# Optimization experiments

Measured on AMD Instinct MI355X. Metric: run time of the kernel, lower is better.

## Reference

```python
import jax, jax.numpy as jnp
import numpy as np

DIM = 512
HEADS = 8
DIM_HEAD = DIM // 8          # 64
INNER = HEADS * DIM_HEAD     # 512
M_LANDMARKS = DIM // 2       # 256
PINV_ITERS = 6
RES_KERNEL = 33
LN_EPS = 1e-5


def setup_inputs() -> dict:
    key = jax.random.key(0)
    ks = jax.random.split(key, 7)
    b, n = 8, 4096
    x = jax.random.normal(ks[0], (b, n, DIM), dtype=jnp.float32)
    gamma = jnp.ones((DIM,), jnp.float32)
    beta = jnp.zeros((DIM,), jnp.float32)
    w_qkv = jax.random.normal(ks[1], (DIM, 3 * INNER), jnp.float32) * 0.02
    w_out = jax.random.normal(ks[2], (INNER, DIM), jnp.float32) * 0.02
    b_out = jnp.zeros((DIM,), jnp.float32)
    # depthwise Conv2d(heads, heads, (33,1), groups=heads): torch weight [H,1,33,1]
    res_kernel = jax.random.normal(ks[3], (HEADS, 1, RES_KERNEL, 1), jnp.float32) * 0.05
    return {"x": x, "gamma": gamma, "beta": beta, "w_qkv": w_qkv,
            "w_out": w_out, "b_out": b_out, "res_kernel": res_kernel}


def _moore_penrose_pinv(a, iters=PINV_ITERS):
    # a: [b, h, m, m]
    abs_a = jnp.abs(a)
    col = abs_a.sum(axis=-1).max()   # global max, as in torch.max(col)
    row = abs_a.sum(axis=-2).max()
    z = jnp.swapaxes(a, -1, -2) / (col * row)
    I = jnp.eye(a.shape[-1], dtype=a.dtype)
    for _ in range(iters):
        az = a @ z
        z = 0.25 * z @ (13. * I - az @ (15. * I - az @ (7. * I - az)))
    return z


def _nystrom_attention(xn, w_qkv, res_kernel, w_out, b_out):
    b, n, _ = xn.shape
    h, dh, m = HEADS, DIM_HEAD, M_LANDMARKS
    scale = dh ** -0.5
    qkv = xn @ w_qkv                               # [b, n, 3*inner]
    q, k, v = jnp.split(qkv, 3, axis=-1)
    def to_heads(t):
        return t.reshape(b, n, h, dh).transpose(0, 2, 1, 3)  # [b,h,n,dh]
    q, k, v = to_heads(q), to_heads(k), to_heads(v)
    q = q * scale

    l = n // m  # n chosen as multiple of m -> no padding branch
    # landmark pooling: '(m l) d -> m d' mean
    q_l = q.reshape(b, h, m, l, dh).mean(axis=3)   # [b,h,m,dh]
    k_l = k.reshape(b, h, m, l, dh).mean(axis=3)

    sim1 = jnp.einsum('bhid,bhjd->bhij', q, k_l)    # [b,h,n,m]
    sim2 = jnp.einsum('bhid,bhjd->bhij', q_l, k_l)  # [b,h,m,m]
    sim3 = jnp.einsum('bhid,bhjd->bhij', q_l, k)    # [b,h,m,n]

    attn1 = jax.nn.softmax(sim1, axis=-1)
    attn2 = jax.nn.softmax(sim2, axis=-1)
    attn3 = jax.nn.softmax(sim3, axis=-1)

    attn2_inv = _moore_penrose_pinv(attn2)
    out = (attn1 @ attn2_inv) @ (attn3 @ v)         # [b,h,n,dh]

    # residual depthwise conv over sequence dim (kernel 33x1, groups=heads)
    pad = RES_KERNEL // 2
    out = out + jax.lax.conv_general_dilated(
        v, res_kernel, window_strides=(1, 1),
        padding=((pad, pad), (0, 0)),
        dimension_numbers=('NCHW', 'OIHW', 'NCHW'),
        feature_group_count=HEADS)

    out = out.transpose(0, 2, 1, 3).reshape(b, n, h * dh)  # [b,n,inner]
    return out @ w_out + b_out  # dropout omitted (eval mode)


def reference(x, gamma, beta, w_qkv, w_out, b_out, res_kernel):
    mu = x.mean(axis=-1, keepdims=True)
    var = x.var(axis=-1, keepdims=True)
    xn = (x - mu) * jax.lax.rsqrt(var + LN_EPS) * gamma + beta
    return x + _nystrom_attention(xn, w_qkv, res_kernel, w_out, b_out)
```

## Files before the change

kernel.cpp:

```cpp
#include <hip/hip_runtime.h>

#define SEQ 4096
#define DMODEL 512
#define NH 8
#define DH 64
#define MLM 256
#define NBH 64
#define NROWS 32768

typedef unsigned short bf16_t;
typedef __attribute__((ext_vector_type(8))) short bf16x8;
typedef __attribute__((ext_vector_type(4))) float f32x4;

__device__ __forceinline__ float bf2f(unsigned short u) {
  return __uint_as_float(((unsigned)u) << 16);
}
__device__ __forceinline__ unsigned short f2bf(float f) {
  unsigned u = __float_as_uint(f);
  u += 0x7fffu + ((u >> 16) & 1u);
  return (unsigned short)(u >> 16);
}
__device__ __forceinline__ void unp8(const bf16_t* p, float* d) {
  uint4 u = *(const uint4*)p;
  d[0] = __uint_as_float(u.x << 16); d[1] = __uint_as_float(u.x & 0xffff0000u);
  d[2] = __uint_as_float(u.y << 16); d[3] = __uint_as_float(u.y & 0xffff0000u);
  d[4] = __uint_as_float(u.z << 16); d[5] = __uint_as_float(u.z & 0xffff0000u);
  d[6] = __uint_as_float(u.w << 16); d[7] = __uint_as_float(u.w & 0xffff0000u);
}

__device__ __forceinline__ void gll(const void* g, void* l) {
  __builtin_amdgcn_global_load_lds(
      (const __attribute__((address_space(1))) unsigned int*)g,
      (__attribute__((address_space(3))) unsigned int*)l, 16, 0, 0);
}

__global__ __launch_bounds__(64) void ln_kernel(const float* __restrict__ x,
    const float* __restrict__ gamma, const float* __restrict__ beta,
    bf16_t* __restrict__ xn) {
  int row = blockIdx.x;
  const float4* xr = (const float4*)(x + (size_t)row * DMODEL);
  int t = threadIdx.x;
  float4 a = xr[t], b = xr[t + 64];
  float s  = a.x + a.y + a.z + a.w + b.x + b.y + b.z + b.w;
  float ss = a.x*a.x + a.y*a.y + a.z*a.z + a.w*a.w
           + b.x*b.x + b.y*b.y + b.z*b.z + b.w*b.w;
#pragma unroll
  for (int off = 32; off > 0; off >>= 1) {
    s  += __shfl_xor(s, off);
    ss += __shfl_xor(ss, off);
  }
  float mean = s * (1.0f / DMODEL);
  float var  = ss * (1.0f / DMODEL) - mean * mean;
  float rstd = rsqrtf(var + 1e-5f);
  const float4* g4 = (const float4*)gamma;
  const float4* be4 = (const float4*)beta;
  ushort4* o = (ushort4*)(xn + (size_t)row * DMODEL);
  float4 g = g4[t], bb = be4[t];
  ushort4 r;
  r.x = f2bf((a.x - mean) * rstd * g.x + bb.x);
  r.y = f2bf((a.y - mean) * rstd * g.y + bb.y);
  r.z = f2bf((a.z - mean) * rstd * g.z + bb.z);
  r.w = f2bf((a.w - mean) * rstd * g.w + bb.w);
  o[t] = r;
  g = g4[t + 64]; bb = be4[t + 64];
  r.x = f2bf((b.x - mean) * rstd * g.x + bb.x);
  r.y = f2bf((b.y - mean) * rstd * g.y + bb.y);
  r.z = f2bf((b.z - mean) * rstd * g.z + bb.z);
  r.w = f2bf((b.w - mean) * rstd * g.w + bb.w);
  o[t + 64] = r;
}

__global__ __launch_bounds__(256) void convT(const float* __restrict__ w,
    bf16_t* __restrict__ wt, int K, int N) {
  size_t idx = (size_t)blockIdx.x * 256 + threadIdx.x;
  int n = (int)(idx / K), k = (int)(idx % K);
  wt[idx] = f2bf(w[(size_t)k * N + n]);
}

#define MFMA_GEMM_BODY(APTR, BTPTR, KDIM) \
  __shared__ short As[128][32]; \
  __shared__ short Bs[128][32]; \
  int tid = threadIdx.x; \
  int lane = tid & 63; \
  int wv = tid >> 6; \
  int wm = (wv & 1) << 6, wn = (wv >> 1) << 6; \
  int l15 = lane & 15, l16 = lane >> 4; \
  f32x4 acc[4][4]; \
  _Pragma("unroll") for (int fm = 0; fm < 4; ++fm) \
    _Pragma("unroll") for (int fn = 0; fn < 4; ++fn) \
      acc[fm][fn] = (f32x4){0.f, 0.f, 0.f, 0.f}; \
  int ar0 = tid >> 2, ac0 = (tid & 3) << 3; \
  const bf16_t* Ab  = (APTR) + (size_t)(m0 + ar0) * (KDIM) + ac0; \
  const bf16_t* Ab1 = (APTR) + (size_t)(m0 + ar0 + 64) * (KDIM) + ac0; \
  const bf16_t* Bb  = (BTPTR) + (size_t)(n0 + ar0) * (KDIM) + ac0; \
  const bf16_t* Bb1 = (BTPTR) + (size_t)(n0 + ar0 + 64) * (KDIM) + ac0; \
  short* AsW  = &As[(wv << 4)][0]; \
  short* AsW1 = &As[64 + (wv << 4)][0]; \
  short* BsW  = &Bs[(wv << 4)][0]; \
  short* BsW1 = &Bs[64 + (wv << 4)][0]; \
  for (int k0 = 0; k0 < (KDIM); k0 += 32) { \
    gll(Ab + k0, AsW);  gll(Ab1 + k0, AsW1); \
    gll(Bb + k0, BsW);  gll(Bb1 + k0, BsW1); \
    __syncthreads(); \
    bf16x8 af[4], bfr[4]; \
    _Pragma("unroll") for (int f = 0; f < 4; ++f) { \
      af[f]  = *(const bf16x8*)&As[wm + f * 16 + l15][l16 * 8]; \
      bfr[f] = *(const bf16x8*)&Bs[wn + f * 16 + l15][l16 * 8]; \
    } \
    _Pragma("unroll") for (int fm = 0; fm < 4; ++fm) \
      _Pragma("unroll") for (int fn = 0; fn < 4; ++fn) \
        acc[fm][fn] = __builtin_amdgcn_mfma_f32_16x16x32_bf16(af[fm], bfr[fn], acc[fm][fn], 0, 0, 0); \
    __syncthreads(); \
  }

__global__ __launch_bounds__(512) void gemm_qkv_256(const bf16_t* __restrict__ A,
    const bf16_t* __restrict__ BT, bf16_t* __restrict__ q, bf16_t* __restrict__ k,
    bf16_t* __restrict__ vT, bf16_t* __restrict__ qlb, bf16_t* __restrict__ klb) {
  int bid = blockIdx.x;
  int orig = (bid & 7) * 96 + (bid >> 3);
  int n0 = (orig % 6) << 8;
  int m0 = (orig / 6) << 8;
  __shared__ short As[4][8192];
  __shared__ short Bs[4][8192];
  int tid = threadIdx.x;
  int lane = tid & 63;
  int wid = tid >> 6;
  int wr = wid >> 2, wc = wid & 3;
  int l15 = lane & 15, l16 = lane >> 4;
  int sl = (l16 ^ (l15 & 3)) << 3;
  int gr  = lane >> 2;
  int gcs = ((lane & 3) ^ ((lane >> 2) & 3)) << 3;
  f32x4 acc[8][4];
#pragma unroll
  for (int fm = 0; fm < 8; ++fm)
#pragma unroll
    for (int fn = 0; fn < 4; ++fn) acc[fm][fn] = (f32x4){0.f, 0.f, 0.f, 0.f};

#define STAGE(kt, s) { \
    _Pragma("unroll") for (int u = 0; u < 2; ++u) { \
      int r0 = (wid << 5) + (u << 4); \
      gll(A  + (size_t)(m0 + r0 + gr) * 512 + (kt) * 32 + gcs, &As[s][r0 << 5]); \
      gll(BT + (size_t)(n0 + r0 + gr) * 512 + (kt) * 32 + gcs, &Bs[s][r0 << 5]); \
    } }

  STAGE(0, 0) STAGE(1, 1) STAGE(2, 2)
  for (int t = 0; t < 16; ++t) {
    int s = t & 3;
    if (t < 14)       asm volatile("s_waitcnt vmcnt(8)" ::: "memory");
    else if (t == 14) asm volatile("s_waitcnt vmcnt(4)" ::: "memory");
    else              asm volatile("s_waitcnt vmcnt(0)" ::: "memory");
    __builtin_amdgcn_s_barrier();
    if (t + 3 < 16) STAGE(t + 3, ((t + 3) & 3))
    bf16x8 a[8], b[4];
#pragma unroll
    for (int fm = 0; fm < 8; ++fm)
      a[fm] = *(const bf16x8*)&As[s][(((wr << 7) + (fm << 4) + l15) << 5) + sl];
#pragma unroll
    for (int fn = 0; fn < 4; ++fn)
      b[fn] = *(const bf16x8*)&Bs[s][(((wc << 6) + (fn << 4) + l15) << 5) + sl];
    asm volatile("s_waitcnt lgkmcnt(0)" ::: "memory");
    __builtin_amdgcn_sched_barrier(0);
    __builtin_amdgcn_s_setprio(1);
#pragma unroll
    for (int fm = 0; fm < 8; ++fm)
#pragma unroll
      for (int fn = 0; fn < 4; ++fn)
        acc[fm][fn] = __builtin_amdgcn_mfma_f32_16x16x32_bf16(a[fm], b[fn], acc[fm][fn], 0, 0, 0);
    __builtin_amdgcn_s_setprio(0);
  }
#undef STAGE
#pragma unroll
  for (int fm = 0; fm < 8; ++fm) {
    int row0 = m0 + (wr << 7) + (fm << 4) + (l16 << 2);
    int bat = row0 >> 12;
    int nn0 = row0 & 4095;
    int lm  = nn0 >> 4;
#pragma unroll
    for (int fn = 0; fn < 4; ++fn) {
      int col = n0 + (wc << 6) + (fn << 4) + l15;
      int which = col >> 9;
      int hd = (col >> 6) & 7;
      int d  = col & 63;
      if (which == 2) {
        ushort4 pk;
        pk.x = f2bf(acc[fm][fn][0]); pk.y = f2bf(acc[fm][fn][1]);
        pk.z = f2bf(acc[fm][fn][2]); pk.w = f2bf(acc[fm][fn][3]);
        *(ushort4*)(vT + ((size_t)(bat * NH + hd) * DH + d) * SEQ + nn0) = pk;
      } else {
        bf16_t* dst = (which == 0) ? q : k;
        float scale = (which == 0) ? 0.125f : 1.f;
#pragma unroll
        for (int rg = 0; rg < 4; ++rg)
          dst[(((size_t)(bat * NH + hd)) * SEQ + nn0 + rg) * DH + d] = f2bf(acc[fm][fn][rg] * scale);
        float s = acc[fm][fn][0] + acc[fm][fn][1] + acc[fm][fn][2] + acc[fm][fn][3];
        s += __shfl_xor(s, 16);
        s += __shfl_xor(s, 32);
        if (l16 == 0) {
          bf16_t* pdst = (which == 0) ? qlb : klb;
          pdst[((size_t)(bat * NH + hd) * MLM + lm) * DH + d] = f2bf(s * scale * 0.0625f);
        }
      }
    }
  }
}

__global__ __launch_bounds__(256) void gemm_out_mfma(const bf16_t* __restrict__ A,
    const bf16_t* __restrict__ BT, const float* __restrict__ bias,
    const float* __restrict__ x, float* __restrict__ y) {
  int bid = blockIdx.x;
  int orig = (bid & 7) * 128 + (bid >> 3);
  int n0 = (orig & 3) << 7;
  int m0 = (orig >> 2) << 7;
  MFMA_GEMM_BODY(A, BT, 512)
#pragma unroll
  for (int fm = 0; fm < 4; ++fm) {
#pragma unroll
    for (int fn = 0; fn < 4; ++fn) {
      int col = n0 + wn + fn * 16 + l15;
      float bv = bias[col];
#pragma unroll
      for (int rg = 0; rg < 4; ++rg) {
        int row = m0 + wm + fm * 16 + l16 * 4 + rg;
        y[(size_t)row * DMODEL + col] = x[(size_t)row * DMODEL + col] + acc[fm][fn][rg] + bv;
      }
    }
  }
}

__global__ __launch_bounds__(256) void bmm_mfma32(const bf16_t* __restrict__ Ag,
    const bf16_t* __restrict__ BTg, bf16_t* __restrict__ Cb,
    bf16_t* __restrict__ CTb, float* __restrict__ Cf,
    int K, float alpha, float eA, float diagc, int flags) {
  int bid = blockIdx.x;
  int orig = (bid & 7) * 512 + (bid >> 3);
  int bh = orig >> 6;
  int tile = orig & 63;
  int n0 = (tile & 7) << 5;
  int m0 = (tile >> 3) << 5;
  const bf16_t* A  = Ag + (size_t)bh * 256 * K;
  const bf16_t* BT = BTg + (size_t)bh * 256 * K;
  __shared__ short As[32][264];
  __shared__ short Bs[32][264];
  int tid = threadIdx.x;
  int lane = tid & 63;
  int wv = tid >> 6;
  int wm = (wv & 1) << 4, wn = (wv >> 1) << 4;
  int l15 = lane & 15, l16 = lane >> 4;
  int ar0 = tid >> 3, ac0 = (tid & 7) << 2;
  const bf16_t* Ab = A + (size_t)(m0 + ar0) * K + ac0;
  const bf16_t* Bb = BT + (size_t)(n0 + ar0) * K + ac0;
  int nch = K >> 5;
  uint2 ga[8], gb[8];
#pragma unroll 8
  for (int u = 0; u < 8; ++u)
    if (u < nch) { ga[u] = *(const uint2*)(Ab + u * 32); gb[u] = *(const uint2*)(Bb + u * 32); }
#pragma unroll 8
  for (int u = 0; u < 8; ++u)
    if (u < nch) { *(uint2*)&As[ar0][ac0 + u * 32] = ga[u]; *(uint2*)&Bs[ar0][ac0 + u * 32] = gb[u]; }
  __syncthreads();
  f32x4 acc = (f32x4){0.f, 0.f, 0.f, 0.f};
#pragma unroll 8
  for (int u = 0; u < 8; ++u)
    if (u < nch) {
      bf16x8 af = *(const bf16x8*)&As[wm + l15][u * 32 + l16 * 8];
      bf16x8 bf = *(const bf16x8*)&Bs[wn + l15][u * 32 + l16 * 8];
      acc = __builtin_amdgcn_mfma_f32_16x16x32_bf16(af, bf, acc, 0, 0, 0);
    }
  size_t cbase = (size_t)bh * 65536;
  int row0 = m0 + wm + l16 * 4;
  int col = n0 + wn + l15;
  float v4[4];
#pragma unroll
  for (int rg = 0; rg < 4; ++rg) {
    float val = alpha * acc[rg];
    if (eA != 0.f) val += eA * bf2f(A[(size_t)(row0 + rg) * K + col]);
    if (row0 + rg == col) val += diagc;
    v4[rg] = val;
  }
  if (flags & 1) {
#pragma unroll
    for (int rg = 0; rg < 4; ++rg)
      Cb[cbase + (size_t)(row0 + rg) * 256 + col] = f2bf(v4[rg]);
  }
  if (flags & 2) {
    ushort4 pk;
    pk.x = f2bf(v4[0]); pk.y = f2bf(v4[1]);
    pk.z = f2bf(v4[2]); pk.w = f2bf(v4[3]);
    *(ushort4*)(CTb + cbase + (size_t)col * 256 + row0) = pk;
  }
  if (flags & 4) {
#pragma unroll
    for (int rg = 0; rg < 4; ++rg)
      Cf[cbase + (size_t)(row0 + rg) * 256 + col] = v4[rg];
  }
}

__global__ __launch_bounds__(256) void ns_zy32(const bf16_t* __restrict__ zg,
    const bf16_t* __restrict__ Yg, const bf16_t* __restrict__ t1Tg,
    bf16_t* __restrict__ zog, bf16_t* __restrict__ Yog,
    bf16_t* __restrict__ YTog) {
  int bid = blockIdx.x;
  int orig = (bid & 7) * 1024 + (bid >> 3);
  int task = orig >> 6;
  int bh = task >> 1;
  int which = task & 1;
  int tile = orig & 63;
  int n0 = (tile & 7) << 5;
  int m0 = (tile >> 3) << 5;
  const bf16_t* A  = (which ? Yg : zg) + ((size_t)bh << 16);
  const bf16_t* BT = t1Tg + ((size_t)bh << 16);
  __shared__ short As[32][264];
  __shared__ short Bs[32][264];
  int tid = threadIdx.x;
  int lane = tid & 63;
  int wv = tid >> 6;
  int wm = (wv & 1) << 4, wn = (wv >> 1) << 4;
  int l15 = lane & 15, l16 = lane >> 4;
  int ar0 = tid >> 3, ac0 = (tid & 7) << 2;
  const bf16_t* Ab = A + (size_t)(m0 + ar0) * 256 + ac0;
  const bf16_t* Bb = BT + (size_t)(n0 + ar0) * 256 + ac0;
  uint2 ga[8], gb[8];
#pragma unroll
  for (int u = 0; u < 8; ++u) {
    ga[u] = *(const uint2*)(Ab + u * 32);
    gb[u] = *(const uint2*)(Bb + u * 32);
  }
#pragma unroll
  for (int u = 0; u < 8; ++u) {
    *(uint2*)&As[ar0][ac0 + u * 32] = ga[u];
    *(uint2*)&Bs[ar0][ac0 + u * 32] = gb[u];
  }
  __syncthreads();
  f32x4 acc = (f32x4){0.f, 0.f, 0.f, 0.f};
#pragma unroll
  for (int u = 0; u < 8; ++u) {
    bf16x8 af = *(const bf16x8*)&As[wm + l15][u * 32 + l16 * 8];
    bf16x8 bf = *(const bf16x8*)&Bs[wn + l15][u * 32 + l16 * 8];
    acc = __builtin_amdgcn_mfma_f32_16x16x32_bf16(af, bf, acc, 0, 0, 0);
  }
  size_t cbase = (size_t)bh << 16;
  int row0 = m0 + wm + l16 * 4;
  int col = n0 + wn + l15;
  float v4[4];
#pragma unroll
  for (int rg = 0; rg < 4; ++rg) v4[rg] = 0.25f * acc[rg];
  if (which == 0) {
#pragma unroll
    for (int rg = 0; rg < 4; ++rg)
      zog[cbase + (size_t)(row0 + rg) * 256 + col] = f2bf(v4[rg]);
  } else {
#pragma unroll
    for (int rg = 0; rg < 4; ++rg)
      Yog[cbase + (size_t)(row0 + rg) * 256 + col] = f2bf(v4[rg]);
    ushort4 pk;
    pk.x = f2bf(v4[0]); pk.y = f2bf(v4[1]);
    pk.z = f2bf(v4[2]); pk.w = f2bf(v4[3]);
    *(ushort4*)(YTog + cbase + (size_t)col * 256 + row0) = pk;
  }
}

__global__ __launch_bounds__(256) void softmax256(const float* __restrict__ af,
    bf16_t* __restrict__ ab) {
  const float* ar = af + (size_t)blockIdx.x * MLM;
  int t = threadIdx.x;
  float v = ar[t];
  __shared__ float redm[4], reds[4];
  float m = v;
#pragma unroll
  for (int off = 32; off > 0; off >>= 1) m = fmaxf(m, __shfl_xor(m, off));
  if ((t & 63) == 0) redm[t >> 6] = m;
  __syncthreads();
  m = fmaxf(fmaxf(redm[0], redm[1]), fmaxf(redm[2], redm[3]));
  float p = __expf(v - m);
  float s = p;
#pragma unroll
  for (int off = 32; off > 0; off >>= 1) s += __shfl_xor(s, off);
  if ((t & 63) == 0) reds[t >> 6] = s;
  __syncthreads();
  s = reds[0] + reds[1] + reds[2] + reds[3];
  ab[(size_t)blockIdx.x * MLM + t] = f2bf(p / s);
}

__global__ void init_scal(unsigned* s) { if (threadIdx.x < 2) s[threadIdx.x] = 0u; }

__global__ __launch_bounds__(256) void colrow_max(const bf16_t* __restrict__ a,
    unsigned* __restrict__ scal) {
  int bh = blockIdx.x;
  int task = blockIdx.y;
  const bf16_t* ab = a + (size_t)bh * MLM * MLM;
  int t = threadIdx.x;
  float s = 0.f;
  if (task == 0) {
    const bf16_t* rp = ab + (size_t)t * MLM;
    for (int j = 0; j < MLM; j += 8) {
      float d[8];
      unp8(rp + j, d);
      s += d[0]; s += d[1]; s += d[2]; s += d[3];
      s += d[4]; s += d[5]; s += d[6]; s += d[7];
    }
  } else {
    for (int i = 0; i < MLM; ++i) s += bf2f(ab[(size_t)i * MLM + t]);
  }
  __shared__ float red[4];
  float m = s;
#pragma unroll
  for (int off = 32; off > 0; off >>= 1) m = fmaxf(m, __shfl_xor(m, off));
  if ((t & 63) == 0) red[t >> 6] = m;
  __syncthreads();
  if (t == 0) {
    m = fmaxf(fmaxf(red[0], red[1]), fmaxf(red[2], red[3]));
    atomicMax(scal + task, __float_as_uint(m));
  }
}

__global__ __launch_bounds__(256) void zinit(const bf16_t* __restrict__ ab,
    bf16_t* __restrict__ z0, bf16_t* __restrict__ z0T,
    const unsigned* __restrict__ scal) {
  size_t idx = (size_t)blockIdx.x * 256 + threadIdx.x;
  float denom = __uint_as_float(scal[0]) * __uint_as_float(scal[1]);
  size_t bh = idx >> 16;
  int i = (int)((idx >> 8) & 255);
  int j = (int)(idx & 255);
  bf16_t r = f2bf(bf2f(ab[idx]) / denom);
  z0T[idx] = r;
  z0[(bh << 16) + ((size_t)j << 8) + i] = r;
}

__global__ __launch_bounds__(64) void attn3v_mfma(const bf16_t* __restrict__ qlb,
    const bf16_t* __restrict__ kg, const bf16_t* __restrict__ vT,
    float* __restrict__ pacc, float* __restrict__ pm, float* __restrict__ ps) {
  int bid = blockIdx.x;
  int orig = (bid & 7) * 512 + (bid >> 3);
  int m0 = (orig & 7) << 5;
  int cz = (orig >> 3) & 7;
  int bh = orig >> 6;
  int lane = threadIdx.x;
  int l15 = lane & 15, l16 = lane >> 4;
  __shared__ short plds[32][136];
  const bf16_t* qbase = qlb + (size_t)bh * MLM * DH;
  const bf16_t* kbase = kg + (size_t)bh * SEQ * DH;
  const bf16_t* vbase = vT + (size_t)bh * DH * SEQ;
  bf16x8 af[2][2];
#pragma unroll
  for (int mt = 0; mt < 2; ++mt)
#pragma unroll
    for (int ks = 0; ks < 2; ++ks)
      af[mt][ks] = *(const bf16x8*)(qbase + (size_t)(m0 + mt * 16 + l15) * DH + ks * 32 + l16 * 8);
  float m_run[2][4], s_run[2][4];
  f32x4 o[2][4];
#pragma unroll
  for (int mt = 0; mt < 2; ++mt) {
#pragma unroll
    for (int rg = 0; rg < 4; ++rg) { m_run[mt][rg] = -1e30f; s_run[mt][rg] = 0.f; }
#pragma unroll
    for (int n2 = 0; n2 < 4; ++n2) o[mt][n2] = (f32x4){0.f, 0.f, 0.f, 0.f};
  }
  int kbeg = cz << 9;
  for (int kt = kbeg; kt < kbeg + 512; kt += 128) {
    f32x4 sacc[2][8];
#pragma unroll
    for (int mt = 0; mt < 2; ++mt)
#pragma unroll
      for (int nt = 0; nt < 8; ++nt) sacc[mt][nt] = (f32x4){0.f, 0.f, 0.f, 0.f};
#pragma unroll
    for (int nt = 0; nt < 8; ++nt) {
      const bf16_t* kr = kbase + (size_t)(kt + nt * 16 + l15) * DH + l16 * 8;
      bf16x8 b0 = *(const bf16x8*)kr;
      bf16x8 b1 = *(const bf16x8*)(kr + 32);
      sacc[0][nt] = __builtin_amdgcn_mfma_f32_16x16x32_bf16(af[0][0], b0, sacc[0][nt], 0, 0, 0);
      sacc[0][nt] = __builtin_amdgcn_mfma_f32_16x16x32_bf16(af[0][1], b1, sacc[0][nt], 0, 0, 0);
      sacc[1][nt] = __builtin_amdgcn_mfma_f32_16x16x32_bf16(af[1][0], b0, sacc[1][nt], 0, 0, 0);
      sacc[1][nt] = __builtin_amdgcn_mfma_f32_16x16x32_bf16(af[1][1], b1, sacc[1][nt], 0, 0, 0);
    }
#pragma unroll
    for (int mt = 0; mt < 2; ++mt)
#pragma unroll
      for (int rg = 0; rg < 4; ++rg) {
        float mx = sacc[mt][0][rg];
#pragma unroll
        for (int nt = 1; nt < 8; ++nt) mx = fmaxf(mx, sacc[mt][nt][rg]);
        mx = fmaxf(mx, __shfl_xor(mx, 1));
        mx = fmaxf(mx, __shfl_xor(mx, 2));
        mx = fmaxf(mx, __shfl_xor(mx, 4));
        mx = fmaxf(mx, __shfl_xor(mx, 8));
        float mnew = fmaxf(m_run[mt][rg], mx);
        float corr = __expf(m_run[mt][rg] - mnew);
        float s = 0.f;
#pragma unroll
        for (int nt = 0; nt < 8; ++nt) {
          float p = __expf(sacc[mt][nt][rg] - mnew);
          sacc[mt][nt][rg] = p;
          s += p;
        }
        s += __shfl_xor(s, 1); s += __shfl_xor(s, 2);
        s += __shfl_xor(s, 4); s += __shfl_xor(s, 8);
        s_run[mt][rg] = s_run[mt][rg] * corr + s;
        m_run[mt][rg] = mnew;
#pragma unroll
        for (int n2 = 0; n2 < 4; ++n2) o[mt][n2][rg] *= corr;
      }
#pragma unroll
    for (int mt = 0; mt < 2; ++mt)
#pragma unroll
      for (int nt = 0; nt < 8; ++nt)
#pragma unroll
        for (int rg = 0; rg < 4; ++rg)
          plds[mt * 16 + l16 * 4 + rg][nt * 16 + l15] = (short)f2bf(sacc[mt][nt][rg]);
#pragma unroll
    for (int ks2 = 0; ks2 < 4; ++ks2) {
      bf16x8 pa0 = *(const bf16x8*)&plds[l15][ks2 * 32 + l16 * 8];
      bf16x8 pa1 = *(const bf16x8*)&plds[16 + l15][ks2 * 32 + l16 * 8];
#pragma unroll
      for (int n2 = 0; n2 < 4; ++n2) {
        bf16x8 vb8 = *(const bf16x8*)(vbase + (size_t)(n2 * 16 + l15) * SEQ + kt + ks2 * 32 + l16 * 8);
        o[0][n2] = __builtin_amdgcn_mfma_f32_16x16x32_bf16(pa0, vb8, o[0][n2], 0, 0, 0);
        o[1][n2] = __builtin_amdgcn_mfma_f32_16x16x32_bf16(pa1, vb8, o[1][n2], 0, 0, 0);
      }
    }
  }
  size_t pidx0 = (size_t)(bh * 8 + cz) * MLM + m0;
#pragma unroll
  for (int mt = 0; mt < 2; ++mt)
#pragma unroll
    for (int n2 = 0; n2 < 4; ++n2)
#pragma unroll
      for (int rg = 0; rg < 4; ++rg) {
        int row = mt * 16 + l16 * 4 + rg;
        pacc[(pidx0 + row) * 64 + n2 * 16 + l15] = o[mt][n2][rg];
      }
  if (l15 == 0) {
#pragma unroll
    for (int mt = 0; mt < 2; ++mt)
#pragma unroll
      for (int rg = 0; rg < 4; ++rg) {
        pm[pidx0 + mt * 16 + l16 * 4 + rg] = m_run[mt][rg];
        ps[pidx0 + mt * 16 + l16 * 4 + rg] = s_run[mt][rg];
      }
  }
}

__global__ __launch_bounds__(256) void attn3v_comb(const float* __restrict__ pacc,
    const float* __restrict__ pm, const float* __restrict__ ps,
    bf16_t* __restrict__ a3vb) {
  int gw = blockIdx.x * 4 + (threadIdx.x >> 6);
  int lane = threadIdx.x & 63;
  int bh = gw >> 8, row = gw & 255;
  float ms[8];
  float M = -1e30f;
#pragma unroll
  for (int cc = 0; cc < 8; ++cc) {
    ms[cc] = pm[(size_t)(bh * 8 + cc) * MLM + row];
    M = fmaxf(M, ms[cc]);
  }
  float S = 0.f, val = 0.f;
#pragma unroll
  for (int cc = 0; cc < 8; ++cc) {
    size_t pidx = (size_t)(bh * 8 + cc) * MLM + row;
    float w = __expf(ms[cc] - M);
    S += w * ps[pidx];
    val += w * pacc[pidx * 64 + lane];
  }
  a3vb[(size_t)gw * 64 + lane] = f2bf(val / S);
}

__global__ __launch_bounds__(256) void wm_kernel(const bf16_t* __restrict__ zb,
    const bf16_t* __restrict__ a3vb, bf16_t* __restrict__ wmT) {
  int bh = blockIdx.y;
  int m0 = blockIdx.x << 6;
  __shared__ bf16_t a3s[MLM * DH];
  int t = threadIdx.x;
  const bf16_t* asrc = a3vb + (size_t)bh * MLM * DH;
#pragma unroll
  for (int i = 0; i < 8; ++i)
    *(bf16x8*)(a3s + ((size_t)t + 256 * i) * 8) =
        *(const bf16x8*)(asrc + ((size_t)t + 256 * i) * 8);
  __syncthreads();
  int row = m0 + (t >> 2);
  int c0 = (t & 3) * 16;
  const bf16_t* zrow = zb + (size_t)bh * 65536 + (size_t)row * 256;
  float acc16[16] = {};
  for (int k0 = 0; k0 < 256; k0 += 8) {
    float a8[8];
    unp8(zrow + k0, a8);
#pragma unroll
    for (int j = 0; j < 8; ++j) {
      float av[16];
      unp8(a3s + (k0 + j) * 64 + c0, av);
      unp8(a3s + (k0 + j) * 64 + c0 + 8, av + 8);
#pragma unroll
      for (int e = 0; e < 16; ++e) acc16[e] += a8[j] * av[e];
    }
  }
  bf16_t* wd = wmT + (size_t)bh * DH * MLM;
#pragma unroll
  for (int e = 0; e < 16; ++e)
    wd[(size_t)(c0 + e) * MLM + row] = f2bf(acc16[e]);
}

__global__ __launch_bounds__(64) void attn1_mfma(const bf16_t* __restrict__ qg,
    const bf16_t* __restrict__ klb, const bf16_t* __restrict__ wmT,
    bf16_t* __restrict__ om) {
  int bh = blockIdx.y, bat = bh >> 3, head = bh & 7;
  int m0 = blockIdx.x << 5;
  int lane = threadIdx.x;
  int l15 = lane & 15, l16 = lane >> 4;
  __shared__ short plds[32][264];
  const bf16_t* qbase = qg + (size_t)bh * SEQ * DH;
  const bf16_t* kbase = klb + (size_t)bh * MLM * DH;
  bf16x8 af[2][2];
#pragma unroll
  for (int mt = 0; mt < 2; ++mt)
#pragma unroll
    for (int ks = 0; ks < 2; ++ks)
      af[mt][ks] = *(const bf16x8*)(qbase + (size_t)(m0 + mt * 16 + l15) * DH + ks * 32 + l16 * 8);
  f32x4 acc[2][16];
#pragma unroll
  for (int mt = 0; mt < 2; ++mt)
#pragma unroll
    for (int nt = 0; nt < 16; ++nt) acc[mt][nt] = (f32x4){0.f, 0.f, 0.f, 0.f};
#pragma unroll
  for (int nt = 0; nt < 16; ++nt) {
    bf16x8 b0 = *(const bf16x8*)(kbase + (size_t)(nt * 16 + l15) * DH + l16 * 8);
    bf16x8 b1 = *(const bf16x8*)(kbase + (size_t)(nt * 16 + l15) * DH + 32 + l16 * 8);
    acc[0][nt] = __builtin_amdgcn_mfma_f32_16x16x32_bf16(af[0][0], b0, acc[0][nt], 0, 0, 0);
    acc[0][nt] = __builtin_amdgcn_mfma_f32_16x16x32_bf16(af[0][1], b1, acc[0][nt], 0, 0, 0);
    acc[1][nt] = __builtin_amdgcn_mfma_f32_16x16x32_bf16(af[1][0], b0, acc[1][nt], 0, 0, 0);
    acc[1][nt] = __builtin_amdgcn_mfma_f32_16x16x32_bf16(af[1][1], b1, acc[1][nt], 0, 0, 0);
  }
  float inv[2][4];
#pragma unroll
  for (int mt = 0; mt < 2; ++mt)
#pragma unroll
    for (int rg = 0; rg < 4; ++rg) {
      float mx = acc[mt][0][rg];
#pragma unroll
      for (int nt = 1; nt < 16; ++nt) mx = fmaxf(mx, acc[mt][nt][rg]);
      mx = fmaxf(mx, __shfl_xor(mx, 1));
      mx = fmaxf(mx, __shfl_xor(mx, 2));
      mx = fmaxf(mx, __shfl_xor(mx, 4));
      mx = fmaxf(mx, __shfl_xor(mx, 8));
      float s = 0.f;
#pragma unroll
      for (int nt = 0; nt < 16; ++nt) {
        float p = __expf(acc[mt][nt][rg] - mx);
        acc[mt][nt][rg] = p;
        s += p;
      }
      s += __shfl_xor(s, 1); s += __shfl_xor(s, 2);
      s += __shfl_xor(s, 4); s += __shfl_xor(s, 8);
      inv[mt][rg] = 1.f / s;
    }
#pragma unroll
  for (int mt = 0; mt < 2; ++mt)
#pragma unroll
    for (int nt = 0; nt < 16; ++nt)
#pragma unroll
      for (int rg = 0; rg < 4; ++rg)
        plds[mt * 16 + l16 * 4 + rg][nt * 16 + l15] = (short)f2bf(acc[mt][nt][rg]);
  const bf16_t* wbase = wmT + (size_t)bh * DH * MLM;
  f32x4 o[2][4];
#pragma unroll
  for (int mt = 0; mt < 2; ++mt)
#pragma unroll
    for (int n2 = 0; n2 < 4; ++n2) o[mt][n2] = (f32x4){0.f, 0.f, 0.f, 0.f};
#pragma unroll
  for (int ks = 0; ks < 8; ++ks) {
    bf16x8 pa0 = *(const bf16x8*)&plds[l15][ks * 32 + l16 * 8];
    bf16x8 pa1 = *(const bf16x8*)&plds[16 + l15][ks * 32 + l16 * 8];
#pragma unroll
    for (int n2 = 0; n2 < 4; ++n2) {
      bf16x8 wb = *(const bf16x8*)(wbase + (size_t)(n2 * 16 + l15) * MLM + ks * 32 + l16 * 8);
      o[0][n2] = __builtin_amdgcn_mfma_f32_16x16x32_bf16(pa0, wb, o[0][n2], 0, 0, 0);
      o[1][n2] = __builtin_amdgcn_mfma_f32_16x16x32_bf16(pa1, wb, o[1][n2], 0, 0, 0);
    }
  }
#pragma unroll
  for (int mt = 0; mt < 2; ++mt)
#pragma unroll
    for (int n2 = 0; n2 < 4; ++n2)
#pragma unroll
      for (int rg = 0; rg < 4; ++rg) {
        int n = m0 + mt * 16 + l16 * 4 + rg;
        int d = n2 * 16 + l15;
        om[((size_t)(bat * SEQ + n)) * DMODEL + head * DH + d] =
            f2bf(o[mt][n2][rg] * inv[mt][rg]);
      }
}

__global__ __launch_bounds__(256) void conv_add(const bf16_t* __restrict__ vT,
    const float* __restrict__ rk, bf16_t* __restrict__ om) {
  int bh = blockIdx.y, bat = bh >> 3, head = bh & 7;
  int n0 = blockIdx.x << 5;
  __shared__ bf16_t vs[64 * 64];
  int t = threadIdx.x;
  int d = t & 63;
  int nq = (t >> 6) << 4;
  const bf16_t* vrow = vT + ((size_t)bh * DH + d) * SEQ;
#pragma unroll
  for (int h = 0; h < 2; ++h) {
    int nb = n0 - 16 + nq + h * 8;
    unsigned short tmp[8];
    if (nb >= 0 && nb + 8 <= SEQ) {
      bf16x8 val = *(const bf16x8*)(vrow + nb);
#pragma unroll
      for (int e = 0; e < 8; ++e) tmp[e] = ((unsigned short*)&val)[e];
    } else {
#pragma unroll
      for (int e = 0; e < 8; ++e) {
        int n = nb + e;
        tmp[e] = (n >= 0 && n < SEQ) ? vrow[n] : (unsigned short)0;
      }
    }
#pragma unroll
    for (int e = 0; e < 8; ++e) vs[(nq + h * 8 + e) * 64 + d] = tmp[e];
  }
  __syncthreads();
  float w[33];
#pragma unroll
  for (int i = 0; i < 33; ++i) w[i] = rk[head * 33 + i];
  int r0 = (t >> 6) << 3;
  float out[8] = {0.f, 0.f, 0.f, 0.f, 0.f, 0.f, 0.f, 0.f};
#pragma unroll
  for (int j = 0; j < 40; ++j) {
    float vv = bf2f(vs[(r0 + j) * 64 + d]);
    int ilo = j - 32; if (ilo < 0) ilo = 0;
    int ihi = j; if (ihi > 7) ihi = 7;
    for (int i = ilo; i <= ihi; ++i) out[i] += w[j - i] * vv;
  }
#pragma unroll
  for (int i = 0; i < 8; ++i) {
    int n = n0 + r0 + i;
    size_t idx = ((size_t)(bat * SEQ + n)) * DMODEL + head * DH + d;
    om[idx] = f2bf(bf2f(om[idx]) + out[i]);
  }
}

extern "C" void kernel_launch(void* const* d_in, const int* in_sizes, int n_in,
                              void* d_out, int out_size, void* d_ws, size_t ws_size,
                              hipStream_t stream) {
  const float* x     = (const float*)d_in[0];
  const float* gamma = (const float*)d_in[1];
  const float* beta  = (const float*)d_in[2];
  const float* w_qkv = (const float*)d_in[3];
  const float* w_out = (const float*)d_in[4];
  const float* b_out = (const float*)d_in[5];
  const float* rk    = (const float*)d_in[6];
  float* y  = (float*)d_out;

  bf16_t* xnb  = (bf16_t*)d_ws;
  bf16_t* qb   = xnb + 16777216;
  bf16_t* kb   = qb + 16777216;
  bf16_t* vTb  = kb + 16777216;
  bf16_t* wqkvT = vTb + 16777216;
  bf16_t* woutT = wqkvT + 786432;
  bf16_t* qlb  = woutT + 262144;
  bf16_t* klb  = qlb + 1048576;
  bf16_t* a2b  = klb + 1048576;
  bf16_t* zA   = a2b + 4194304;
  bf16_t* z0T  = zA + 4194304;
  bf16_t* zB   = z0T + 4194304;
  bf16_t* Ya   = zB + 4194304;
  bf16_t* Yb   = z0T;
  bf16_t* a3vb = Ya + 4194304;
  bf16_t* wmT  = a3vb + 1048576;
  float*  SR   = (float*)(wmT + 1048576);
  float*  a2f  = SR;
  float*  pacc = SR;
  bf16_t* YTa  = (bf16_t*)SR;
  bf16_t* YTb  = YTa + 4194304;
  bf16_t* t2T  = YTa + 8388608;
  bf16_t* t1T  = YTa + 12582912;
  float*  pm   = SR + 8388608;
  float*  ps   = pm + 131072;
  unsigned* scal = (unsigned*)(ps + 131072);
  size_t need = (size_t)93323264 * 2 + (size_t)(8388608 + 262144) * 4 + 64;
  if (ws_size < need) return;

  ln_kernel<<<NROWS, 64, 0, stream>>>(x, gamma, beta, xnb);
  convT<<<3072, 256, 0, stream>>>(w_qkv, wqkvT, 512, 1536);
  convT<<<1024, 256, 0, stream>>>(w_out, woutT, 512, 512);

  gemm_qkv_256<<<768, 512, 0, stream>>>(xnb, wqkvT, qb, kb, vTb, qlb, klb);

  bmm_mfma32<<<4096, 256, 0, stream>>>(qlb, klb, nullptr, nullptr, a2f,
      64, 1.f, 0.f, 0.f, 4);
  softmax256<<<NBH * MLM, 256, 0, stream>>>(a2f, a2b);

  init_scal<<<1, 64, 0, stream>>>(scal);
  colrow_max<<<dim3(NBH, 2), 256, 0, stream>>>(a2b, scal);

  attn3v_mfma<<<4096, 64, 0, stream>>>(qlb, kb, vTb, pacc, pm, ps);
  attn3v_comb<<<4096, 256, 0, stream>>>(pacc, pm, ps, a3vb);

  zinit<<<16384, 256, 0, stream>>>(a2b, zA, z0T, scal);
  bmm_mfma32<<<4096, 256, 0, stream>>>(a2b, z0T, Ya, YTa, nullptr,
      256, 1.f, 0.f, 0.f, 3);
  bf16_t* zc = zA;  bf16_t* zo = zB;
  bf16_t* Yc = Ya;  bf16_t* YTc = YTa;
  bf16_t* Yo = Yb;  bf16_t* YTo = YTb;
  for (int it = 0; it < 6; ++it) {
    bmm_mfma32<<<4096, 256, 0, stream>>>(Yc, YTc, nullptr, t2T, nullptr,
        256, 1.f, -7.f, 15.f, 2);
    bmm_mfma32<<<4096, 256, 0, stream>>>(Yc, t2T, nullptr, t1T, nullptr,
        256, -1.f, 0.f, 13.f, 2);
    ns_zy32<<<8192, 256, 0, stream>>>(zc, Yc, t1T, zo, Yo, YTo);
    bf16_t* tp;
    tp = zc; zc = zo; zo = tp;
    tp = Yc; Yc = Yo; Yo = tp;
    tp = YTc; YTc = YTo; YTo = tp;
  }

  wm_kernel<<<dim3(4, NBH), 256, 0, stream>>>(zc, a3vb, wmT);

  bf16_t* om = xnb;
  attn1_mfma<<<dim3(SEQ / 32, NBH), 64, 0, stream>>>(qb, klb, wmT, om);
  conv_add<<<dim3(SEQ / 32, NBH), 256, 0, stream>>>(vTb, rk, om);

  gemm_out_mfma<<<1024, 256, 0, stream>>>(om, woutT, b_out, x, y);
}
```

Before: 762.8 us.

## Restructure Newton-Schulz pinv iteration to pair independent GEMMs and defer z update

Rewrites each pseudo-inverse iteration so the Y update is expressed through W=Y·Y and U=7Y−W. The z update from the previous iteration (z·t1) runs alongside W in one launch, and Y·U and Y·U-based t1 run together in a second launch. That gives two launches per iteration instead of three, plus one final z GEMM. It also folds init_scal into the weight transpose kernel and zinit into the attn3v combine kernel to cut launch count. The change alters the bf16 rounding points in the iteration, which may shift numerics slightly.

```diff
diff --git a/kernel.cpp b/kernel.cpp
--- a/kernel.cpp
+++ b/kernel.cpp
@@ -70,11 +70,19 @@
   o[t + 64] = r;
 }
 
-__global__ __launch_bounds__(256) void convT(const float* __restrict__ w,
-    bf16_t* __restrict__ wt, int K, int N) {
+__global__ __launch_bounds__(256) void convT2(const float* __restrict__ wqkv,
+    const float* __restrict__ wout, bf16_t* __restrict__ wqkvT,
+    bf16_t* __restrict__ woutT, unsigned* __restrict__ scal) {
+  if (blockIdx.x == 0 && threadIdx.x < 2) scal[threadIdx.x] = 0u;
   size_t idx = (size_t)blockIdx.x * 256 + threadIdx.x;
-  int n = (int)(idx / K), k = (int)(idx % K);
-  wt[idx] = f2bf(w[(size_t)k * N + n]);
+  if (idx < 786432) {
+    int n = (int)(idx / 512), k = (int)(idx % 512);
+    wqkvT[idx] = f2bf(wqkv[(size_t)k * 1536 + n]);
+  } else {
+    size_t j = idx - 786432;
+    int n = (int)(j / 512), k = (int)(j % 512);
+    woutT[j] = f2bf(wout[(size_t)k * 512 + n]);
+  }
 }
 
 #define MFMA_GEMM_BODY(APTR, BTPTR, KDIM) \
@@ -112,6 +120,29 @@
         acc[fm][fn] = __builtin_amdgcn_mfma_f32_16x16x32_bf16(af[fm], bfr[fn], acc[fm][fn], 0, 0, 0); \
     __syncthreads(); \
   }
+
+#define BMM256_BODY(APTR, BTPTR) \
+  __shared__ short As[32][264]; \
+  __shared__ short Bs[32][264]; \
+  int tid = threadIdx.x; \
+  int lane = tid & 63; \
+  int wv = tid >> 6; \
+  int wm = (wv & 1) << 4, wn = (wv >> 1) << 4; \
+  int l15 = lane & 15, l16 = lane >> 4; \
+  int ar0 = tid >> 3, ac0 = (tid & 7) << 2; \
+  const bf16_t* Ab = (APTR) + (size_t)(m0 + ar0) * 256 + ac0; \
+  const bf16_t* Bb = (BTPTR) + (size_t)(n0 + ar0) * 256 + ac0; \
+  uint2 ga[8], gb[8]; \
+  _Pragma("unroll") for (int u = 0; u < 8; ++u) { \
+    ga[u] = *(const uint2*)(Ab + u * 32); gb[u] = *(const uint2*)(Bb + u * 32); } \
+  _Pragma("unroll") for (int u = 0; u < 8; ++u) { \
+    *(uint2*)&As[ar0][ac0 + u * 32] = ga[u]; *(uint2*)&Bs[ar0][ac0 + u * 32] = gb[u]; } \
+  __syncthreads(); \
+  f32x4 acc = (f32x4){0.f, 0.f, 0.f, 0.f}; \
+  _Pragma("unroll") for (int u = 0; u < 8; ++u) { \
+    bf16x8 af = *(const bf16x8*)&As[wm + l15][u * 32 + l16 * 8]; \
+    bf16x8 bf = *(const bf16x8*)&Bs[wn + l15][u * 32 + l16 * 8]; \
+    acc = __builtin_amdgcn_mfma_f32_16x16x32_bf16(af, bf, acc, 0, 0, 0); }
 
 __global__ __launch_bounds__(512) void gemm_qkv_256(const bf16_t* __restrict__ A,
     const bf16_t* __restrict__ BT, bf16_t* __restrict__ q, bf16_t* __restrict__ k,
@@ -295,67 +326,88 @@
   }
 }
 
-__global__ __launch_bounds__(256) void ns_zy32(const bf16_t* __restrict__ zg,
-    const bf16_t* __restrict__ Yg, const bf16_t* __restrict__ t1Tg,
-    bf16_t* __restrict__ zog, bf16_t* __restrict__ Yog,
-    bf16_t* __restrict__ YTog) {
+__global__ __launch_bounds__(256) void pinv_WU(const bf16_t* __restrict__ Yc,
+    const bf16_t* __restrict__ YTc, const bf16_t* __restrict__ zc,
+    const bf16_t* __restrict__ t1Tp, bf16_t* __restrict__ Wb,
+    bf16_t* __restrict__ UT, bf16_t* __restrict__ zo) {
   int bid = blockIdx.x;
-  int orig = (bid & 7) * 1024 + (bid >> 3);
-  int task = orig >> 6;
-  int bh = task >> 1;
-  int which = task & 1;
-  int tile = orig & 63;
+  int cpx = gridDim.x >> 3;
+  int orig = (bid & 7) * cpx + (bid >> 3);
+  int zt = orig >> 12;
+  int o = orig & 4095;
+  int bh = o >> 6;
+  int tile = o & 63;
   int n0 = (tile & 7) << 5;
   int m0 = (tile >> 3) << 5;
-  const bf16_t* A  = (which ? Yg : zg) + ((size_t)bh << 16);
-  const bf16_t* BT = t1Tg + ((size_t)bh << 16);
-  __shared__ short As[32][264];
-  __shared__ short Bs[32][264];
-  int tid = threadIdx.x;
-  int lane = tid & 63;
-  int wv = tid >> 6;
-  int wm = (wv & 1) << 4, wn = (wv >> 1) << 4;
-  int l15 = lane & 15, l16 = lane >> 4;
-  int ar0 = tid >> 3, ac0 = (tid & 7) << 2;
-  const bf16_t* Ab = A + (size_t)(m0 + ar0) * 256 + ac0;
-  const bf16_t* Bb = BT + (size_t)(n0 + ar0) * 256 + ac0;
-  uint2 ga[8], gb[8];
-#pragma unroll
-  for (int u = 0; u < 8; ++u) {
-    ga[u] = *(const uint2*)(Ab + u * 32);
-    gb[u] = *(const uint2*)(Bb + u * 32);
-  }
-#pragma unroll
-  for (int u = 0; u < 8; ++u) {
-    *(uint2*)&As[ar0][ac0 + u * 32] = ga[u];
-    *(uint2*)&Bs[ar0][ac0 + u * 32] = gb[u];
-  }
-  __syncthreads();
-  f32x4 acc = (f32x4){0.f, 0.f, 0.f, 0.f};
-#pragma unroll
-  for (int u = 0; u < 8; ++u) {
-    bf16x8 af = *(const bf16x8*)&As[wm + l15][u * 32 + l16 * 8];
-    bf16x8 bf = *(const bf16x8*)&Bs[wn + l15][u * 32 + l16 * 8];
-    acc = __builtin_amdgcn_mfma_f32_16x16x32_bf16(af, bf, acc, 0, 0, 0);
-  }
+  const bf16_t* A  = (zt ? zc : Yc) + ((size_t)bh << 16);
+  const bf16_t* BT = (zt ? t1Tp : YTc) + ((size_t)bh << 16);
+  BMM256_BODY(A, BT)
   size_t cbase = (size_t)bh << 16;
   int row0 = m0 + wm + l16 * 4;
   int col = n0 + wn + l15;
-  float v4[4];
-#pragma unroll
-  for (int rg = 0; rg < 4; ++rg) v4[rg] = 0.25f * acc[rg];
-  if (which == 0) {
+  if (zt) {
 #pragma unroll
     for (int rg = 0; rg < 4; ++rg)
-      zog[cbase + (size_t)(row0 + rg) * 256 + col] = f2bf(v4[rg]);
+      zo[cbase + (size_t)(row0 + rg) * 256 + col] = f2bf(0.25f * acc[rg]);
   } else {
-#pragma unroll
-    for (int rg = 0; rg < 4; ++rg)
-      Yog[cbase + (size_t)(row0 + rg) * 256 + col] = f2bf(v4[rg]);
     ushort4 pk;
-    pk.x = f2bf(v4[0]); pk.y = f2bf(v4[1]);
-    pk.z = f2bf(v4[2]); pk.w = f2bf(v4[3]);
-    *(ushort4*)(YTog + cbase + (size_t)col * 256 + row0) = pk;
+    unsigned short uv[4];
+#pragma unroll
+    for (int rg = 0; rg < 4; ++rg) {
+      float w = acc[rg];
+      float y = bf2f(Yc[cbase + (size_t)(row0 + rg) * 256 + col]);
+      Wb[cbase + (size_t)(row0 + rg) * 256 + col] = f2bf(w);
+      uv[rg] = f2bf(7.f * y - w);
+    }
+    pk.x = uv[0]; pk.y = uv[1]; pk.z = uv[2]; pk.w = uv[3];
+    *(ushort4*)(UT + cbase + (size_t)col * 256 + row0) = pk;
+  }
+}
+
+__global__ __launch_bounds__(256) void pinv_E(const bf16_t* __restrict__ Yc,
+    const bf16_t* __restrict__ Wb, const bf16_t* __restrict__ UT,
+    bf16_t* __restrict__ Yo, bf16_t* __restrict__ YTo,
+    bf16_t* __restrict__ t1T) {
+  int bid = blockIdx.x;
+  int orig = (bid & 7) * 1024 + (bid >> 3);
+  int task = orig >> 12;
+  int o = orig & 4095;
+  int bh = o >> 6;
+  int tile = o & 63;
+  int n0 = (tile & 7) << 5;
+  int m0 = (tile >> 3) << 5;
+  const bf16_t* A  = (task ? Yc : Wb) + ((size_t)bh << 16);
+  const bf16_t* BT = UT + ((size_t)bh << 16);
+  BMM256_BODY(A, BT)
+  size_t cbase = (size_t)bh << 16;
+  int row0 = m0 + wm + l16 * 4;
+  int col = n0 + wn + l15;
+  if (task == 0) {
+    ushort4 pk;
+    unsigned short yv[4];
+#pragma unroll
+    for (int rg = 0; rg < 4; ++rg) {
+      size_t idx = cbase + (size_t)(row0 + rg) * 256 + col;
+      float y = bf2f(Yc[idx]);
+      float w = bf2f(Wb[idx]);
+      float v = 0.25f * acc[rg] + 3.25f * y - 3.75f * w;
+      yv[rg] = f2bf(v);
+      Yo[idx] = yv[rg];
+    }
+    pk.x = yv[0]; pk.y = yv[1]; pk.z = yv[2]; pk.w = yv[3];
+    *(ushort4*)(YTo + cbase + (size_t)col * 256 + row0) = pk;
+  } else {
+    ushort4 pk;
+    unsigned short tv[4];
+#pragma unroll
+    for (int rg = 0; rg < 4; ++rg) {
+      float y = bf2f(Yc[cbase + (size_t)(row0 + rg) * 256 + col]);
+      float v = acc[rg] - 15.f * y;
+      if (row0 + rg == col) v += 13.f;
+      tv[rg] = f2bf(v);
+    }
+    pk.x = tv[0]; pk.y = tv[1]; pk.z = tv[2]; pk.w = tv[3];
+    *(ushort4*)(t1T + cbase + (size_t)col * 256 + row0) = pk;
   }
 }
 
@@ -380,8 +432,6 @@
   s = reds[0] + reds[1] + reds[2] + reds[3];
   ab[(size_t)blockIdx.x * MLM + t] = f2bf(p / s);
 }
-
-__global__ void init_scal(unsigned* s) { if (threadIdx.x < 2) s[threadIdx.x] = 0u; }
 
 __global__ __launch_bounds__(256) void colrow_max(const bf16_t* __restrict__ a,
     unsigned* __restrict__ scal) {
@@ -411,19 +461,6 @@
     m = fmaxf(fmaxf(red[0], red[1]), fmaxf(red[2], red[3]));
     atomicMax(scal + task, __float_as_uint(m));
   }
-}
-
-__global__ __launch_bounds__(256) void zinit(const bf16_t* __restrict__ ab,
-    bf16_t* __restrict__ z0, bf16_t* __restrict__ z0T,
-    const unsigned* __restrict__ scal) {
-  size_t idx = (size_t)blockIdx.x * 256 + threadIdx.x;
-  float denom = __uint_as_float(scal[0]) * __uint_as_float(scal[1]);
-  size_t bh = idx >> 16;
-  int i = (int)((idx >> 8) & 255);
-  int j = (int)(idx & 255);
-  bf16_t r = f2bf(bf2f(ab[idx]) / denom);
-  z0T[idx] = r;
-  z0[(bh << 16) + ((size_t)j << 8) + i] = r;
 }
 
 __global__ __launch_bounds__(64) void attn3v_mfma(const bf16_t* __restrict__ qlb,
@@ -539,28 +576,41 @@
   }
 }
 
-__global__ __launch_bounds__(256) void attn3v_comb(const float* __restrict__ pacc,
+__global__ __launch_bounds__(256) void comb_zinit(const float* __restrict__ pacc,
     const float* __restrict__ pm, const float* __restrict__ ps,
-    bf16_t* __restrict__ a3vb) {
-  int gw = blockIdx.x * 4 + (threadIdx.x >> 6);
-  int lane = threadIdx.x & 63;
-  int bh = gw >> 8, row = gw & 255;
-  float ms[8];
-  float M = -1e30f;
-#pragma unroll
-  for (int cc = 0; cc < 8; ++cc) {
-    ms[cc] = pm[(size_t)(bh * 8 + cc) * MLM + row];
-    M = fmaxf(M, ms[cc]);
-  }
-  float S = 0.f, val = 0.f;
-#pragma unroll
-  for (int cc = 0; cc < 8; ++cc) {
-    size_t pidx = (size_t)(bh * 8 + cc) * MLM + row;
-    float w = __expf(ms[cc] - M);
-    S += w * ps[pidx];
-    val += w * pacc[pidx * 64 + lane];
-  }
-  a3vb[(size_t)gw * 64 + lane] = f2bf(val / S);
+    bf16_t* __restrict__ a3vb, const bf16_t* __restrict__ ab,
+    bf16_t* __restrict__ z0, bf16_t* __restrict__ z0T,
+    const unsigned* __restrict__ scal) {
+  if (blockIdx.x < 4096) {
+    int gw = blockIdx.x * 4 + (threadIdx.x >> 6);
+    int lane = threadIdx.x & 63;
+    int bh = gw >> 8, row = gw & 255;
+    float ms[8];
+    float M = -1e30f;
+#pragma unroll
+    for (int cc = 0; cc < 8; ++cc) {
+      ms[cc] = pm[(size_t)(bh * 8 + cc) * MLM + row];
+      M = fmaxf(M, ms[cc]);
+    }
+    float S = 0.f, val = 0.f;
+#pragma unroll
+    for (int cc = 0; cc < 8; ++cc) {
+      size_t pidx = (size_t)(bh * 8 + cc) * MLM + row;
+      float w = __expf(ms[cc] - M);
+      S += w * ps[pidx];
+      val += w * pacc[pidx * 64 + lane];
+    }
+    a3vb[(size_t)gw * 64 + lane] = f2bf(val / S);
+  } else {
+    size_t idx = (size_t)(blockIdx.x - 4096) * 256 + threadIdx.x;
+    float denom = __uint_as_float(scal[0]) * __uint_as_float(scal[1]);
+    size_t bh = idx >> 16;
+    int i = (int)((idx >> 8) & 255);
+    int j = (int)(idx & 255);
+    bf16_t r = f2bf(bf2f(ab[idx]) / denom);
+    z0T[idx] = r;
+    z0[(bh << 16) + ((size_t)j << 8) + i] = r;
+  }
 }
 
 __global__ __launch_bounds__(256) void wm_kernel(const bf16_t* __restrict__ zb,
@@ -768,8 +818,9 @@
   float*  pacc = SR;
   bf16_t* YTa  = (bf16_t*)SR;
   bf16_t* YTb  = YTa + 4194304;
-  bf16_t* t2T  = YTa + 8388608;
+  bf16_t* Wb   = YTa + 8388608;
   bf16_t* t1T  = YTa + 12582912;
+  bf16_t* UT   = xnb;
   float*  pm   = SR + 8388608;
   float*  ps   = pm + 131072;
   unsigned* scal = (unsigned*)(ps + 131072);
@@ -777,38 +828,39 @@
   if (ws_size < need) return;
 
   ln_kernel<<<NROWS, 64, 0, stream>>>(x, gamma, beta, xnb);
-  convT<<<3072, 256, 0, stream>>>(w_qkv, wqkvT, 512, 1536);
-  convT<<<1024, 256, 0, stream>>>(w_out, woutT, 512, 512);
+  convT2<<<4096, 256, 0, stream>>>(w_qkv, w_out, wqkvT, woutT, scal);
 
   gemm_qkv_256<<<768, 512, 0, stream>>>(xnb, wqkvT, qb, kb, vTb, qlb, klb);
 
   bmm_mfma32<<<4096, 256, 0, stream>>>(qlb, klb, nullptr, nullptr, a2f,
       64, 1.f, 0.f, 0.f, 4);
   softmax256<<<NBH * MLM, 256, 0, stream>>>(a2f, a2b);
-
-  init_scal<<<1, 64, 0, stream>>>(scal);
   colrow_max<<<dim3(NBH, 2), 256, 0, stream>>>(a2b, scal);
 
   attn3v_mfma<<<4096, 64, 0, stream>>>(qlb, kb, vTb, pacc, pm, ps);
-  attn3v_comb<<<4096, 256, 0, stream>>>(pacc, pm, ps, a3vb);
-
-  zinit<<<16384, 256, 0, stream>>>(a2b, zA, z0T, scal);
+  comb_zinit<<<20480, 256, 0, stream>>>(pacc, pm, ps, a3vb, a2b, zA, z0T, scal);
+
   bmm_mfma32<<<4096, 256, 0, stream>>>(a2b, z0T, Ya, YTa, nullptr,
       256, 1.f, 0.f, 0.f, 3);
+
   bf16_t* zc = zA;  bf16_t* zo = zB;
   bf16_t* Yc = Ya;  bf16_t* YTc = YTa;
   bf16_t* Yo = Yb;  bf16_t* YTo = YTb;
   for (int it = 0; it < 6; ++it) {
-    bmm_mfma32<<<4096, 256, 0, stream>>>(Yc, YTc, nullptr, t2T, nullptr,
-        256, 1.f, -7.f, 15.f, 2);
-    bmm_mfma32<<<4096, 256, 0, stream>>>(Yc, t2T, nullptr, t1T, nullptr,
-        256, -1.f, 0.f, 13.f, 2);
-    ns_zy32<<<8192, 256, 0, stream>>>(zc, Yc, t1T, zo, Yo, YTo);
+    if (it == 0) {
+      pinv_WU<<<4096, 256, 0, stream>>>(Yc, YTc, nullptr, nullptr, Wb, UT, nullptr);
+    } else {
+      pinv_WU<<<8192, 256, 0, stream>>>(Yc, YTc, zc, t1T, Wb, UT, zo);
+      bf16_t* tp = zc; zc = zo; zo = tp;
+    }
+    pinv_E<<<8192, 256, 0, stream>>>(Yc, Wb, UT, Yo, YTo, t1T);
     bf16_t* tp;
-    tp = zc; zc = zo; zo = tp;
     tp = Yc; Yc = Yo; Yo = tp;
     tp = YTc; YTc = YTo; YTo = tp;
   }
+  bmm_mfma32<<<4096, 256, 0, stream>>>(zc, t1T, zo, nullptr, nullptr,
+      256, 0.25f, 0.f, 0.f, 1);
+  { bf16_t* tp = zc; zc = zo; zo = tp; }
 
   wm_kernel<<<dim3(4, NBH), 256, 0, stream>>>(zc, a3vb, wmT);
 
```

Measured after the change: 760.3 us. Within noise of the previous version (-0.3%).
